# Performance work log

Hardware: AMD Instinct MI355X
Metric: run time of the kernel (lower is better)

## Reference

```python
import jax, jax.numpy as jnp
import numpy as np

H = 32        # num_attention_heads
KVH = 8       # num_key_value_heads
D = 64        # attention_head_size
WIN = 256     # attention_window_size (left/right)
ROPE_BASE = 10000.0


def setup_inputs() -> dict:
    key = jax.random.key(0)
    k1, k2, k3 = jax.random.split(key, 3)
    B, S = 2, 2048
    return {
        "query_states": jax.random.normal(k1, (B, S, H * D), dtype=jnp.float32),
        "key_states": jax.random.normal(k2, (B, S, KVH * D), dtype=jnp.float32),
        "value_states": jax.random.normal(k3, (B, S, KVH * D), dtype=jnp.float32),
    }


def _rope_cos_sin(seq_len, dtype):
    inv_freq = 1.0 / (ROPE_BASE ** (jnp.arange(0, D, 2, dtype=jnp.float32) / D))  # [D/2]
    pos = jnp.arange(seq_len, dtype=jnp.float32)
    freqs = pos[:, None] * inv_freq[None, :]          # [S, D/2]
    emb = jnp.concatenate([freqs, freqs], axis=-1)    # [S, D]
    return jnp.cos(emb).astype(dtype), jnp.sin(emb).astype(dtype)


def _rotate_half(x):
    x1, x2 = x[..., : D // 2], x[..., D // 2 :]
    return jnp.concatenate([-x2, x1], axis=-1)


def reference(query_states, key_states, value_states):
    B, S, _ = query_states.shape
    n_rep = H // KVH

    q = query_states.reshape(B, S, H, D).transpose(0, 2, 1, 3)        # [B,H,S,D]
    k = key_states.reshape(B, S, KVH, D).transpose(0, 2, 1, 3)        # [B,KVH,S,D]
    v = value_states.reshape(B, S, KVH, D).transpose(0, 2, 1, 3)

    # repeat_kv: [B,KVH,S,D] -> [B,H,S,D]
    k = jnp.repeat(k, n_rep, axis=1)
    v = jnp.repeat(v, n_rep, axis=1)

    cos, sin = _rope_cos_sin(S, q.dtype)   # [S,D]
    cos = cos[None, None]                  # [1,1,S,D]
    sin = sin[None, None]
    q = q * cos + _rotate_half(q) * sin
    k = k * cos + _rotate_half(k) * sin

    scale = 1.0 / jnp.sqrt(jnp.asarray(D, dtype=q.dtype))
    scores = jnp.einsum("bhqd,bhkd->bhqk", q, k) * scale              # [B,H,S,S]

    i = jnp.arange(S)[:, None]
    j = jnp.arange(S)[None, :]
    allowed = (j >= i - WIN) & (j <= i)                               # [S,S]
    scores = jnp.where(allowed[None, None], scores, jnp.finfo(scores.dtype).min)

    probs = jax.nn.softmax(scores, axis=-1)
    out = jnp.einsum("bhqk,bhkd->bhqd", probs, v)                     # [B,H,S,D]
    return out.transpose(0, 2, 1, 3).reshape(B, S, H * D)
```

## Files before the change

kernel.cpp:

```cpp
#include <hip/hip_runtime.h>
#include <math.h>

#define NH   32
#define NKVH 8
#define HD   64
#define WIN  256
#define BB   2
#define SS   2048

typedef short short8 __attribute__((ext_vector_type(8)));
typedef float f32x4  __attribute__((ext_vector_type(4)));

__device__ __forceinline__ ushort f2bf(float x) {
    union { float f; unsigned u; } v; v.f = x;
    unsigned u = v.u + 0x7FFF + ((v.u >> 16) & 1);
    return (ushort)(u >> 16);
}

__device__ __forceinline__ int cvtpk_bf16(float lo, float hi) {
    int r;
    asm("v_cvt_pk_bf16_f32 %0, %1, %2" : "=v"(r) : "v"(lo), "v"(hi));
    return r;
}

__device__ __forceinline__ int swz(int L) { return L ^ (((L >> 7) & 7) << 4); }

__device__ __forceinline__ void stage16(const void* g, void* l) {
    __builtin_amdgcn_global_load_lds(
        (const __attribute__((address_space(1))) unsigned int*)g,
        (__attribute__((address_space(3))) unsigned int*)l, 16, 0, 0);
}

__global__ __launch_bounds__(256) void prep_kv(const float* __restrict__ K,
                                               const float* __restrict__ V,
                                               ushort* __restrict__ Kr,
                                               ushort* __restrict__ Vt) {
    __shared__ ushort tile[32][65];
    const int bidx = blockIdx.x;
    const int sblk = bidx & 63;
    const int s0   = sblk * 32;
    const int kvh  = (bidx >> 6) & 7;
    const int b    = bidx >> 9;
    const int d = threadIdx.x & 63, g = threadIdx.x >> 6;

    const float inv = __powf(10000.f, -(float)(d & 31) * (1.f / 32.f));

    float kv[8], vv[8];
#pragma unroll
    for (int i = 0; i < 8; ++i) {
        int s = s0 + g * 8 + i;
        kv[i] = K[(size_t)(b * SS + s) * (NKVH * HD) + kvh * HD + d];
        vv[i] = V[(size_t)(b * SS + s) * (NKVH * HD) + kvh * HD + d];
    }
    char* kc = (char*)(Kr + (size_t)(b * NKVH + kvh) * SS * HD) + (size_t)sblk * 4096;
#pragma unroll
    for (int i = 0; i < 8; ++i) {
        int s  = s0 + g * 8 + i;
        int sl = g * 8 + i;
        float partner = __shfl(kv[i], d ^ 32, 64);
        float sn, cs;
        __sincosf((float)s * inv, &sn, &cs);
        float krot = kv[i] * cs + ((d < 32) ? -partner : partner) * sn;
        *(ushort*)(kc + swz(sl * 128 + d * 2)) = f2bf(krot);
        tile[sl][d] = f2bf(vv[i]);
    }
    __syncthreads();
    char* vc = (char*)(Vt + (size_t)(b * NKVH + kvh) * HD * SS) + (size_t)sblk * 4096;
    const int sl2 = (threadIdx.x & 15) * 2, drg = threadIdx.x >> 4;
#pragma unroll
    for (int i = 0; i < 4; ++i) {
        int dr = drg * 4 + i;
        ushort2 u = make_ushort2(tile[sl2][dr], tile[sl2 + 1][dr]);
        *(ushort2*)(vc + swz(dr * 64 + sl2 * 2)) = u;
    }
}

__global__ __launch_bounds__(256, 4) void attn_mfma(const float* __restrict__ Q,
                                                    const ushort* __restrict__ Kr,
                                                    const ushort* __restrict__ Vt,
                                                    float* __restrict__ O) {
    __shared__ __align__(16) ushort ldsK[2][2048];
    __shared__ __align__(16) ushort ldsV[2][2048];
    const int wv = threadIdx.x >> 6, lane = threadIdx.x & 63;
    const int lo16 = lane & 15, quad = lane >> 4;
    const int bidx = (blockIdx.x & 7) * 128 + (blockIdx.x >> 3);
    const int qblk = bidx & 63;
    const int kvh  = (bidx >> 6) & 7;
    const int b    = bidx >> 9;
    const int h    = kvh * 4 + wv;
    const int q0   = qblk * 32;

    float invf[8];
#pragma unroll
    for (int j = 0; j < 8; ++j)
        invf[j] = __powf(10000.f, -(float)(quad * 8 + j) * (1.f / 32.f));

    short8 aq[2][2];
#pragma unroll
    for (int t = 0; t < 2; ++t) {
        int qi = q0 + t * 16 + lo16;
        const float* qrow = Q + (size_t)(b * SS + qi) * (NH * HD) + h * HD;
        float lo[8], hi[8];
        *(float4*)(lo)     = *(const float4*)(qrow + quad * 8);
        *(float4*)(lo + 4) = *(const float4*)(qrow + quad * 8 + 4);
        *(float4*)(hi)     = *(const float4*)(qrow + 32 + quad * 8);
        *(float4*)(hi + 4) = *(const float4*)(qrow + 32 + quad * 8 + 4);
#pragma unroll
        for (int j = 0; j < 8; ++j) {
            float sn, cs;
            __sincosf((float)qi * invf[j], &sn, &cs);
            aq[t][0][j] = (short)f2bf((lo[j] * cs - hi[j] * sn) * 0.125f);
            aq[t][1][j] = (short)f2bf((hi[j] * cs + lo[j] * sn) * 0.125f);
        }
    }

    const char* kbase = (const char*)(Kr + (size_t)(b * NKVH + kvh) * SS * HD);
    const char* vbase = (const char*)(Vt + (size_t)(b * NKVH + kvh) * HD * SS);

    f32x4 acc[2][4];
#pragma unroll
    for (int t = 0; t < 2; ++t)
#pragma unroll
        for (int i = 0; i < 4; ++i) acc[t][i] = (f32x4){0.f, 0.f, 0.f, 0.f};
    float psum[2] = {0.f, 0.f};

    const int idxAB = (lo16 + ((quad & 1) << 5)) << 2;
    const int idxCD = idxAB + 64;
    const bool hiq  = quad >= 2;

    int klo = q0 - WIN; if (klo < 0) klo = 0;
    const int c0  = klo >> 5;
    const int cnt = (q0 >> 5) - c0 + 1;

    {
        const char* kc = kbase + (size_t)c0 * 4096 + wv * 1024 + lane * 16;
        const char* vc = vbase + (size_t)c0 * 4096 + wv * 1024 + lane * 16;
        stage16(kc, (char*)&ldsK[0][0] + wv * 1024);
        stage16(vc, (char*)&ldsV[0][0] + wv * 1024);
    }
    __syncthreads();

    int nb = 0;
    for (int it = 0; it < cnt; ++it, nb ^= 1) {
        const int kb = klo + it * 32;
        if (it + 1 < cnt) {
            const char* kc = kbase + (size_t)(c0 + it + 1) * 4096 + wv * 1024 + lane * 16;
            const char* vc = vbase + (size_t)(c0 + it + 1) * 4096 + wv * 1024 + lane * 16;
            stage16(kc, (char*)&ldsK[nb ^ 1][0] + wv * 1024);
            stage16(vc, (char*)&ldsV[nb ^ 1][0] + wv * 1024);
        }

        const char* kl = (const char*)&ldsK[nb][0];
        short8 k0 = *(const short8*)(kl + swz(lo16 * 128 + quad * 16));
        short8 k1 = *(const short8*)(kl + swz(lo16 * 128 + 64 + quad * 16));
        short8 k2 = *(const short8*)(kl + swz((lo16 + 16) * 128 + quad * 16));
        short8 k3 = *(const short8*)(kl + swz((lo16 + 16) * 128 + 64 + quad * 16));

        const f32x4 z = {0.f, 0.f, 0.f, 0.f};
        __builtin_amdgcn_s_setprio(1);
        f32x4 s00 = __builtin_amdgcn_mfma_f32_16x16x32_bf16(k0, aq[0][0], z,   0, 0, 0);
        s00       = __builtin_amdgcn_mfma_f32_16x16x32_bf16(k1, aq[0][1], s00, 0, 0, 0);
        f32x4 s01 = __builtin_amdgcn_mfma_f32_16x16x32_bf16(k2, aq[0][0], z,   0, 0, 0);
        s01       = __builtin_amdgcn_mfma_f32_16x16x32_bf16(k3, aq[0][1], s01, 0, 0, 0);
        f32x4 s10 = __builtin_amdgcn_mfma_f32_16x16x32_bf16(k0, aq[1][0], z,   0, 0, 0);
        s10       = __builtin_amdgcn_mfma_f32_16x16x32_bf16(k1, aq[1][1], s10, 0, 0, 0);
        f32x4 s11 = __builtin_amdgcn_mfma_f32_16x16x32_bf16(k2, aq[1][0], z,   0, 0, 0);
        s11       = __builtin_amdgcn_mfma_f32_16x16x32_bf16(k3, aq[1][1], s11, 0, 0, 0);
        __builtin_amdgcn_s_setprio(0);

        short8 ap[2];
#pragma unroll
        for (int t = 0; t < 2; ++t) {
            const f32x4 sa = t ? s10 : s00;
            const f32x4 sb = t ? s11 : s01;
            const int qtmin = q0 + t * 16;
            const int myq   = qtmin + lo16;
            float p[8];
            if ((kb + 31 > qtmin) || (kb < qtmin + 15 - WIN)) {
#pragma unroll
                for (int r = 0; r < 4; ++r) {
                    int key0 = kb + quad * 4 + r;
                    int key1 = key0 + 16;
                    p[r]     = (key0 <= myq && key0 >= myq - WIN) ? __expf(sa[r]) : 0.f;
                    p[4 + r] = (key1 <= myq && key1 >= myq - WIN) ? __expf(sb[r]) : 0.f;
                }
            } else {
#pragma unroll
                for (int r = 0; r < 4; ++r) { p[r] = __expf(sa[r]); p[4 + r] = __expf(sb[r]); }
            }
            psum[t] += ((p[0] + p[1]) + (p[2] + p[3])) + ((p[4] + p[5]) + (p[6] + p[7]));

            int w0 = cvtpk_bf16(p[0], p[1]);
            int w1 = cvtpk_bf16(p[2], p[3]);
            int w2 = cvtpk_bf16(p[4], p[5]);
            int w3 = cvtpk_bf16(p[6], p[7]);
            int a0 = __builtin_amdgcn_ds_bpermute(idxAB, w0);
            int a2 = __builtin_amdgcn_ds_bpermute(idxAB, w2);
            int b1 = __builtin_amdgcn_ds_bpermute(idxAB, w1);
            int b3 = __builtin_amdgcn_ds_bpermute(idxAB, w3);
            int cc0 = __builtin_amdgcn_ds_bpermute(idxCD, w0);
            int cc2 = __builtin_amdgcn_ds_bpermute(idxCD, w2);
            int d1 = __builtin_amdgcn_ds_bpermute(idxCD, w1);
            int d3 = __builtin_amdgcn_ds_bpermute(idxCD, w3);
            union { int i[4]; short8 s; } u;
            u.i[0] = hiq ? a2  : a0;
            u.i[1] = hiq ? b3  : b1;
            u.i[2] = hiq ? cc2 : cc0;
            u.i[3] = hiq ? d3  : d1;
            ap[t] = u.s;
        }

        const char* vl = (const char*)&ldsV[nb][0];
        short8 vf[4];
#pragma unroll
        for (int i = 0; i < 4; ++i)
            vf[i] = *(const short8*)(vl + swz((i * 16 + lo16) * 64 + quad * 16));

        __builtin_amdgcn_s_setprio(1);
#pragma unroll
        for (int i = 0; i < 4; ++i)
            acc[0][i] = __builtin_amdgcn_mfma_f32_16x16x32_bf16(ap[0], vf[i], acc[0][i], 0, 0, 0);
#pragma unroll
        for (int i = 0; i < 4; ++i)
            acc[1][i] = __builtin_amdgcn_mfma_f32_16x16x32_bf16(ap[1], vf[i], acc[1][i], 0, 0, 0);
        __builtin_amdgcn_s_setprio(0);

        __syncthreads();
    }

#pragma unroll
    for (int t = 0; t < 2; ++t) {
        float ps = psum[t];
        ps += __shfl_xor(ps, 16, 64);
        ps += __shfl_xor(ps, 32, 64);
#pragma unroll
        for (int r = 0; r < 4; ++r) {
            float invr = 1.f / __shfl(ps, quad * 4 + r, 16);
            int qr = q0 + t * 16 + quad * 4 + r;
            size_t orow = ((size_t)(b * SS + qr) * NH + h) * HD;
            O[orow + 0 * 16 + lo16] = acc[t][0][r] * invr;
            O[orow + 1 * 16 + lo16] = acc[t][1][r] * invr;
            O[orow + 2 * 16 + lo16] = acc[t][2][r] * invr;
            O[orow + 3 * 16 + lo16] = acc[t][3][r] * invr;
        }
    }
}

__device__ __forceinline__ float wave_sum(float x) {
#pragma unroll
    for (int off = 32; off > 0; off >>= 1) x += __shfl_xor(x, off, 64);
    return x;
}

__global__ __launch_bounds__(256) void attn_scalar(const float* __restrict__ Q,
                                                   const float* __restrict__ K,
                                                   const float* __restrict__ V,
                                                   float* __restrict__ O) {
    int wave = blockIdx.x * 4 + (threadIdx.x >> 6);
    int lane = threadIdx.x & 63;
    int q  = wave % SS;
    int bh = wave / SS;
    int h  = bh % NH;
    int b  = bh / NH;
    int kvh = h >> 2;

    float inv = __powf(10000.f, -(float)(lane & 31) * (1.f / 32.f));
    float sn, cs;
    __sincosf((float)q * inv, &sn, &cs);

    float qv = Q[(size_t)(b * SS + q) * (NH * HD) + h * HD + lane];
    float qpart = __shfl(qv, lane ^ 32, 64);
    float qrot = (qv * cs + ((lane < 32) ? -qpart : qpart) * sn) * 0.125f;

    const float* vbase = V + (size_t)b * SS * (NKVH * HD) + kvh * HD;
    float m = -1e30f, l = 0.f, acc = 0.f;
    int k0 = q - WIN; if (k0 < 0) k0 = 0;
    for (int k = k0; k <= q; ++k) {
        float kraw = K[(size_t)(b * SS + k) * (NKVH * HD) + kvh * HD + lane];
        float kpart = __shfl(kraw, lane ^ 32, 64);
        float ksn, kcs;
        __sincosf((float)k * inv, &ksn, &kcs);
        float kv = kraw * kcs + ((lane < 32) ? -kpart : kpart) * ksn;
        float vv = vbase[(size_t)k * (NKVH * HD) + lane];
        float score = wave_sum(qrot * kv);
        float mnew  = fmaxf(m, score);
        float alpha = __expf(m - mnew);
        float p     = __expf(score - mnew);
        l   = l * alpha + p;
        acc = acc * alpha + p * vv;
        m   = mnew;
    }
    O[(((size_t)(b * SS + q) * NH) + h) * HD + lane] = acc / l;
}

extern "C" void kernel_launch(void* const* d_in, const int* in_sizes, int n_in,
                              void* d_out, int out_size, void* d_ws, size_t ws_size,
                              hipStream_t stream) {
    const float* Q = (const float*)d_in[0];
    const float* K = (const float*)d_in[1];
    const float* V = (const float*)d_in[2];
    float* O = (float*)d_out;

    size_t kv_elems = (size_t)BB * NKVH * SS * HD;
    size_t need = 2 * kv_elems * sizeof(ushort);

    if (ws_size >= need) {
        ushort* Kr = (ushort*)d_ws;
        ushort* Vt = Kr + kv_elems;
        prep_kv<<<BB * NKVH * (SS / 32), 256, 0, stream>>>(K, V, Kr, Vt);
        attn_mfma<<<BB * NKVH * (SS / 32), 256, 0, stream>>>(Q, Kr, Vt, O);
    } else {
        attn_scalar<<<(BB * NH * SS) / 4, 256, 0, stream>>>(Q, K, V, O);
    }
}
```

Baseline: 114.8 us.

## Fuse K/V RoPE and bf16 conversion into the attention kernel

Removes the separate prep_kv kernel and its bf16 workspace. The attention kernel now loads fp32 K/V chunks from global memory into registers, applies RoPE to K and transposes V, converts both to bf16, and writes them into double-buffered LDS. The global loads for the next chunk are issued before the current chunk's compute, and the LDS writes happen after it. This drops one kernel launch and the workspace round trip, but every block now redoes RoPE for up to 9 KV chunks, adds register pressure, and reads the fp32 inputs instead of the compact bf16 copy. The scalar fallback path is removed.

After: 154.0 us. +34.1%, slower.

```diff
diff --git a/kernel.cpp b/kernel.cpp
--- a/kernel.cpp
+++ b/kernel.cpp
@@ -25,63 +25,14 @@
 
 __device__ __forceinline__ int swz(int L) { return L ^ (((L >> 7) & 7) << 4); }
 
-__device__ __forceinline__ void stage16(const void* g, void* l) {
-    __builtin_amdgcn_global_load_lds(
-        (const __attribute__((address_space(1))) unsigned int*)g,
-        (__attribute__((address_space(3))) unsigned int*)l, 16, 0, 0);
-}
-
-__global__ __launch_bounds__(256) void prep_kv(const float* __restrict__ K,
-                                               const float* __restrict__ V,
-                                               ushort* __restrict__ Kr,
-                                               ushort* __restrict__ Vt) {
-    __shared__ ushort tile[32][65];
-    const int bidx = blockIdx.x;
-    const int sblk = bidx & 63;
-    const int s0   = sblk * 32;
-    const int kvh  = (bidx >> 6) & 7;
-    const int b    = bidx >> 9;
-    const int d = threadIdx.x & 63, g = threadIdx.x >> 6;
-
-    const float inv = __powf(10000.f, -(float)(d & 31) * (1.f / 32.f));
-
-    float kv[8], vv[8];
-#pragma unroll
-    for (int i = 0; i < 8; ++i) {
-        int s = s0 + g * 8 + i;
-        kv[i] = K[(size_t)(b * SS + s) * (NKVH * HD) + kvh * HD + d];
-        vv[i] = V[(size_t)(b * SS + s) * (NKVH * HD) + kvh * HD + d];
-    }
-    char* kc = (char*)(Kr + (size_t)(b * NKVH + kvh) * SS * HD) + (size_t)sblk * 4096;
-#pragma unroll
-    for (int i = 0; i < 8; ++i) {
-        int s  = s0 + g * 8 + i;
-        int sl = g * 8 + i;
-        float partner = __shfl(kv[i], d ^ 32, 64);
-        float sn, cs;
-        __sincosf((float)s * inv, &sn, &cs);
-        float krot = kv[i] * cs + ((d < 32) ? -partner : partner) * sn;
-        *(ushort*)(kc + swz(sl * 128 + d * 2)) = f2bf(krot);
-        tile[sl][d] = f2bf(vv[i]);
-    }
-    __syncthreads();
-    char* vc = (char*)(Vt + (size_t)(b * NKVH + kvh) * HD * SS) + (size_t)sblk * 4096;
-    const int sl2 = (threadIdx.x & 15) * 2, drg = threadIdx.x >> 4;
-#pragma unroll
-    for (int i = 0; i < 4; ++i) {
-        int dr = drg * 4 + i;
-        ushort2 u = make_ushort2(tile[sl2][dr], tile[sl2 + 1][dr]);
-        *(ushort2*)(vc + swz(dr * 64 + sl2 * 2)) = u;
-    }
-}
-
-__global__ __launch_bounds__(256, 4) void attn_mfma(const float* __restrict__ Q,
-                                                    const ushort* __restrict__ Kr,
-                                                    const ushort* __restrict__ Vt,
-                                                    float* __restrict__ O) {
+__global__ __launch_bounds__(256, 4) void attn_fused(const float* __restrict__ Q,
+                                                     const float* __restrict__ K,
+                                                     const float* __restrict__ V,
+                                                     float* __restrict__ O) {
     __shared__ __align__(16) ushort ldsK[2][2048];
     __shared__ __align__(16) ushort ldsV[2][2048];
-    const int wv = threadIdx.x >> 6, lane = threadIdx.x & 63;
+    const int tid = threadIdx.x;
+    const int wv = tid >> 6, lane = tid & 63;
     const int lo16 = lane & 15, quad = lane >> 4;
     const int bidx = (blockIdx.x & 7) * 128 + (blockIdx.x >> 3);
     const int qblk = bidx & 63;
@@ -89,6 +40,45 @@
     const int b    = bidx >> 9;
     const int h    = kvh * 4 + wv;
     const int q0   = qblk * 32;
+
+    const int skey = tid >> 3, sdg = tid & 7;
+    const int skp  = tid & 15, sdq = tid >> 4;
+    const float kratio = 0.74989420933f;
+    const float kinv0  = __powf(10000.f, -(float)((sdg & 3) * 8) * (1.f / 32.f));
+
+    float kx[8]; float4 va, vc;
+#define LOADCHUNK(cidx) do {                                                          \
+        const float* krow_ = K + (size_t)(b * SS + (cidx) * 32 + skey) * (NKVH * HD)  \
+                               + kvh * HD + sdg * 8;                                  \
+        *(float4*)(kx)     = *(const float4*)(krow_);                                 \
+        *(float4*)(kx + 4) = *(const float4*)(krow_ + 4);                             \
+        const float* vrow_ = V + (size_t)(b * SS + (cidx) * 32 + 2 * skp) * (NKVH * HD)\
+                               + kvh * HD + sdq * 4;                                  \
+        va = *(const float4*)(vrow_);                                                 \
+        vc = *(const float4*)(vrow_ + NKVH * HD);                                     \
+    } while (0)
+
+#define ROPEWRITE(kb_, buf_) do {                                                     \
+        int s_ = (kb_) + skey;                                                        \
+        float inv_ = kinv0;                                                           \
+        ushort out_[8];                                                               \
+        _Pragma("unroll")                                                             \
+        for (int j = 0; j < 8; ++j) {                                                 \
+            float partner_ = __shfl(kx[j], (tid & 63) ^ 4, 64);           \
+            float sn_, cs_;                                                           \
+            __sincosf((float)s_ * inv_, &sn_, &cs_);                                  \
+            out_[j] = f2bf(kx[j] * cs_ + ((sdg < 4) ? -partner_ : partner_) * sn_);   \
+            inv_ *= kratio;                                                           \
+        }                                                                             \
+        *(short8*)((char*)&ldsK[buf_][0] + swz(skey * 128 + sdg * 16)) = *(short8*)out_;\
+        _Pragma("unroll")                                                             \
+        for (int j = 0; j < 4; ++j) {                                                 \
+            int d_ = sdq * 4 + j;                                                     \
+            unsigned w_ = (unsigned)f2bf(((const float*)&va)[j])                      \
+                        | ((unsigned)f2bf(((const float*)&vc)[j]) << 16);             \
+            *(unsigned*)((char*)&ldsV[buf_][0] + swz(d_ * 64 + skp * 4)) = w_;        \
+        }                                                                             \
+    } while (0)
 
     float invf[8];
 #pragma unroll
@@ -114,9 +104,6 @@
         }
     }
 
-    const char* kbase = (const char*)(Kr + (size_t)(b * NKVH + kvh) * SS * HD);
-    const char* vbase = (const char*)(Vt + (size_t)(b * NKVH + kvh) * HD * SS);
-
     f32x4 acc[2][4];
 #pragma unroll
     for (int t = 0; t < 2; ++t)
@@ -132,23 +119,14 @@
     const int c0  = klo >> 5;
     const int cnt = (q0 >> 5) - c0 + 1;
 
-    {
-        const char* kc = kbase + (size_t)c0 * 4096 + wv * 1024 + lane * 16;
-        const char* vc = vbase + (size_t)c0 * 4096 + wv * 1024 + lane * 16;
-        stage16(kc, (char*)&ldsK[0][0] + wv * 1024);
-        stage16(vc, (char*)&ldsV[0][0] + wv * 1024);
-    }
+    LOADCHUNK(c0);
+    ROPEWRITE(klo, 0);
     __syncthreads();
 
     int nb = 0;
     for (int it = 0; it < cnt; ++it, nb ^= 1) {
         const int kb = klo + it * 32;
-        if (it + 1 < cnt) {
-            const char* kc = kbase + (size_t)(c0 + it + 1) * 4096 + wv * 1024 + lane * 16;
-            const char* vc = vbase + (size_t)(c0 + it + 1) * 4096 + wv * 1024 + lane * 16;
-            stage16(kc, (char*)&ldsK[nb ^ 1][0] + wv * 1024);
-            stage16(vc, (char*)&ldsV[nb ^ 1][0] + wv * 1024);
-        }
+        if (it + 1 < cnt) LOADCHUNK(c0 + it + 1);
 
         const char* kl = (const char*)&ldsK[nb][0];
         short8 k0 = *(const short8*)(kl + swz(lo16 * 128 + quad * 16));
@@ -225,6 +203,8 @@
             acc[1][i] = __builtin_amdgcn_mfma_f32_16x16x32_bf16(ap[1], vf[i], acc[1][i], 0, 0, 0);
         __builtin_amdgcn_s_setprio(0);
 
+        if (it + 1 < cnt) ROPEWRITE(kb + 32, nb ^ 1);
+
         __syncthreads();
     }
 
@@ -244,53 +224,8 @@
             O[orow + 3 * 16 + lo16] = acc[t][3][r] * invr;
         }
     }
-}
-
-__device__ __forceinline__ float wave_sum(float x) {
-#pragma unroll
-    for (int off = 32; off > 0; off >>= 1) x += __shfl_xor(x, off, 64);
-    return x;
-}
-
-__global__ __launch_bounds__(256) void attn_scalar(const float* __restrict__ Q,
-                                                   const float* __restrict__ K,
-                                                   const float* __restrict__ V,
-                                                   float* __restrict__ O) {
-    int wave = blockIdx.x * 4 + (threadIdx.x >> 6);
-    int lane = threadIdx.x & 63;
-    int q  = wave % SS;
-    int bh = wave / SS;
-    int h  = bh % NH;
-    int b  = bh / NH;
-    int kvh = h >> 2;
-
-    float inv = __powf(10000.f, -(float)(lane & 31) * (1.f / 32.f));
-    float sn, cs;
-    __sincosf((float)q * inv, &sn, &cs);
-
-    float qv = Q[(size_t)(b * SS + q) * (NH * HD) + h * HD + lane];
-    float qpart = __shfl(qv, lane ^ 32, 64);
-    float qrot = (qv * cs + ((lane < 32) ? -qpart : qpart) * sn) * 0.125f;
-
-    const float* vbase = V + (size_t)b * SS * (NKVH * HD) + kvh * HD;
-    float m = -1e30f, l = 0.f, acc = 0.f;
-    int k0 = q - WIN; if (k0 < 0) k0 = 0;
-    for (int k = k0; k <= q; ++k) {
-        float kraw = K[(size_t)(b * SS + k) * (NKVH * HD) + kvh * HD + lane];
-        float kpart = __shfl(kraw, lane ^ 32, 64);
-        float ksn, kcs;
-        __sincosf((float)k * inv, &ksn, &kcs);
-        float kv = kraw * kcs + ((lane < 32) ? -kpart : kpart) * ksn;
-        float vv = vbase[(size_t)k * (NKVH * HD) + lane];
-        float score = wave_sum(qrot * kv);
-        float mnew  = fmaxf(m, score);
-        float alpha = __expf(m - mnew);
-        float p     = __expf(score - mnew);
-        l   = l * alpha + p;
-        acc = acc * alpha + p * vv;
-        m   = mnew;
-    }
-    O[(((size_t)(b * SS + q) * NH) + h) * HD + lane] = acc / l;
+#undef LOADCHUNK
+#undef ROPEWRITE
 }
 
 extern "C" void kernel_launch(void* const* d_in, const int* in_sizes, int n_in,
@@ -300,16 +235,7 @@
     const float* K = (const float*)d_in[1];
     const float* V = (const float*)d_in[2];
     float* O = (float*)d_out;
-
-    size_t kv_elems = (size_t)BB * NKVH * SS * HD;
-    size_t need = 2 * kv_elems * sizeof(ushort);
-
-    if (ws_size >= need) {
-        ushort* Kr = (ushort*)d_ws;
-        ushort* Vt = Kr + kv_elems;
-        prep_kv<<<BB * NKVH * (SS / 32), 256, 0, stream>>>(K, V, Kr, Vt);
-        attn_mfma<<<BB * NKVH * (SS / 32), 256, 0, stream>>>(Q, Kr, Vt, O);
-    } else {
-        attn_scalar<<<(BB * NH * SS) / 4, 256, 0, stream>>>(Q, K, V, O);
-    }
-}
+    (void)d_ws; (void)ws_size;
+
+    attn_fused<<<BB * NKVH * (SS / 32), 256, 0, stream>>>(Q, K, V, O);
+}
```
